# Optimization experiments

Hardware: AMD Instinct MI355X
Metric: run time of the kernel (lower is better)

Reference implementation:

```python
import jax, jax.numpy as jnp
import numpy as np


def setup_inputs() -> dict:
    key = jax.random.key(0)
    ks = jax.random.split(key, 6)
    B, C, H, W = 8, 64, 64, 64
    E = C // 8  # embedding_channels = inChannels // k
    inp = {
        "x": jax.random.normal(ks[0], (B, C, H, W), dtype=jnp.float32),
        "Wk": jax.random.normal(ks[1], (E, C), dtype=jnp.float32) * 0.1,
        "bk": jnp.zeros((E,), dtype=jnp.float32),
        "Wq": jax.random.normal(ks[2], (E, C), dtype=jnp.float32) * 0.1,
        "bq": jnp.zeros((E,), dtype=jnp.float32),
        "Wv": jax.random.normal(ks[3], (E, C), dtype=jnp.float32) * 0.1,
        "bv": jnp.zeros((E,), dtype=jnp.float32),
        "Wo": jax.random.normal(ks[4], (C, E), dtype=jnp.float32) * 0.1,
        "bo": jnp.zeros((C,), dtype=jnp.float32),
        "gamma": jnp.zeros((1,), dtype=jnp.float32),
    }
    return inp


def reference(x, Wk, bk, Wq, bq, Wv, bv, Wo, bo, gamma):
    B, C, H, W = x.shape
    N = H * W
    xf = x.reshape(B, C, N)  # [B, C, N]
    # 1x1 convs are per-pixel linear projections
    f = jnp.einsum('ec,bcn->ben', Wk, xf) + bk[:, None]  # key   [B, E, N]
    g = jnp.einsum('ec,bcn->ben', Wq, xf) + bq[:, None]  # query [B, E, N]
    h = jnp.einsum('ec,bcn->ben', Wv, xf) + bv[:, None]  # value [B, E, N]
    # s = f^T g : [B, N, N]
    s = jnp.einsum('ben,bem->bnm', f, g)
    # softmax over dim=1 (key/row axis) as in the original module
    beta = jax.nn.softmax(s, axis=1)
    v = jnp.einsum('ben,bnm->bem', h, beta)  # [B, E, N]
    o = jnp.einsum('ce,ben->bcn', Wo, v) + bo[:, None]  # [B, C, N]
    o = o.reshape(B, C, H, W)
    y = gamma[0] * o + x
    return (y, o, gamma[0])
```

## Files before the change

### kernel.cpp

```cpp
#include <hip/hip_runtime.h>


#define BB   8
#define CC   64
#define NPIX 4096
#define EE   8
#define BN   (BB*NPIX)
#define YSZ  (BB*CC*NPIX)
#define LOG2E 1.4426950408889634f

typedef __attribute__((ext_vector_type(8))) short bf16x8;
typedef __attribute__((ext_vector_type(4))) float f32x4;

__device__ __forceinline__ unsigned short f2bf_rne(float x) {
    unsigned u = __float_as_uint(x);
    u += 0x7FFFu + ((u >> 16) & 1u);
    return (unsigned short)(u >> 16);
}
__device__ __forceinline__ unsigned pack_bf_trunc(float a, float b) {
    return __builtin_amdgcn_perm(__float_as_uint(b), __float_as_uint(a),
                                 0x07060302u);
}
__device__ __forceinline__ float fexp2(float x) {
    return __int_as_float((int)fmaf(x, 8388608.f, 1065062131.f));
}

__global__ __launch_bounds__(256) void qkv_kernel(
    const float* __restrict__ x,
    const float* __restrict__ Wk, const float* __restrict__ bk,
    const float* __restrict__ Wq, const float* __restrict__ bq,
    const float* __restrict__ Wv, const float* __restrict__ bv,
    unsigned short* __restrict__ QT, unsigned short* __restrict__ KT,
    unsigned short* __restrict__ VT)
{
    const int proj = blockIdx.y;
    const float* W    = (proj == 0) ? Wq : (proj == 1) ? Wk : Wv;
    const float* bias = (proj == 0) ? bq : (proj == 1) ? bk : bv;

    const int bm = blockIdx.x*256 + threadIdx.x;
    const int b  = bm >> 12;
    const int n  = bm & (NPIX-1);
    const float* xb = x + (size_t)b*CC*NPIX + n;

    float xv[CC];
    #pragma unroll
    for (int c = 0; c < CC; ++c) xv[c] = xb[(size_t)c*NPIX];

    float f[EE];
    #pragma unroll
    for (int e = 0; e < EE; ++e) {
        float acc = bias[e];
        #pragma unroll
        for (int c = 0; c < CC; ++c) acc = fmaf(W[e*CC+c], xv[c], acc);
        f[e] = acc;
    }

    if (proj == 0) {
        union { unsigned short s[8]; uint4 v; } t;
        #pragma unroll
        for (int e = 0; e < EE; ++e) t.s[e] = f2bf_rne(f[e] * LOG2E);
        *(uint4*)(QT + (size_t)bm*EE) = t.v;
    } else if (proj == 1) {
        union { unsigned short s[8]; uint4 v; } t;
        #pragma unroll
        for (int e = 0; e < EE; ++e) t.s[e] = f2bf_rne(f[e]);
        *(uint4*)(KT + (size_t)bm*EE) = t.v;
    } else {
        const int p   = n >> 5;
        const int c   = n & 31;
        const int off = ((c & 15) >> 2)*8 + ((c >> 4) << 2) + (c & 3);
        unsigned short* vp = VT + ((size_t)(b*128 + p)*16)*32 + off;
        #pragma unroll
        for (int e = 0; e < EE; ++e) vp[e*32] = f2bf_rne(f[e]);
        vp[8*32] = 0x3F80;
    }
}

__global__ __launch_bounds__(256, 2) void attn_fused(
    const unsigned short* __restrict__ QT, const unsigned short* __restrict__ KT,
    const unsigned short* __restrict__ VT,
    const float* __restrict__ x, const float* __restrict__ Wo,
    const float* __restrict__ bo, const float* __restrict__ gamma,
    float* __restrict__ out)
{
    __shared__ float OB[3*4*256];
    __shared__ float VL[64*13];
    __shared__ float Wos[CC*9];
    __shared__ float bos[CC];

    const int tid  = threadIdx.x;
    const int wave = tid >> 6, lane = tid & 63;
    const int quad = lane >> 4, lm = lane & 15;
    const int b  = blockIdx.x >> 6;
    const int m0 = (blockIdx.x & 63) * 64;

    for (int i = tid; i < CC*EE; i += 256) Wos[(i>>3)*9 + (i&7)] = Wo[i];
    if (tid < CC) bos[tid] = bo[tid];

    const bf16x8 kz = {0,0,0,0,0,0,0,0};
    bf16x8 qf[4][4];
    #pragma unroll
    for (int t = 0; t < 4; ++t) {
        bf16x8 qt = *(const bf16x8*)(QT + (size_t)(b*NPIX + m0 + 16*t + lm)*EE);
        #pragma unroll
        for (int g = 0; g < 4; ++g) qf[t][g] = (quad == g) ? qt : kz;
    }

    f32x4 oacc[4];
    #pragma unroll
    for (int t = 0; t < 4; ++t) oacc[t] = (f32x4){0.f,0.f,0.f,0.f};
    const f32x4 zc = {0.f,0.f,0.f,0.f};

    const unsigned short* Kb = KT + (size_t)b*NPIX*EE;
    const int n_start = wave*1024;
    const unsigned short* kl = Kb + (size_t)(n_start + lane)*EE;
    const int lmv = (lm < 9) ? lm : 8;
    const unsigned short* vl = VT + ((size_t)(b*128 + (n_start >> 5))*16 + lmv)*32
                                  + quad*8;

    bf16x8 kfa  = *(const bf16x8*)(kl);
    bf16x8 vf0a = *(const bf16x8*)(vl);
    bf16x8 vf1a = *(const bf16x8*)(vl + 512);
    bf16x8 kfb  = *(const bf16x8*)(kl + 64*EE);
    bf16x8 vf0b = *(const bf16x8*)(vl + 1024);
    bf16x8 vf1b = *(const bf16x8*)(vl + 1536);
    kl += 128*EE; vl += 2048;

    for (int ch = 0; ch < 16; ++ch) {
        bf16x8 kf = kfa, vf0 = vf0a, vf1 = vf1a;
        kfa = kfb; vf0a = vf0b; vf1a = vf1b;
        if (ch < 14) {
            kfb  = *(const bf16x8*)(kl);
            vf0b = *(const bf16x8*)(vl);
            vf1b = *(const bf16x8*)(vl + 512);
            kl += 64*EE; vl += 1024;
        }

        #pragma unroll
        for (int t = 0; t < 4; ++t) {
            f32x4 s0 = __builtin_amdgcn_mfma_f32_16x16x32_bf16(kf, qf[t][0], zc, 0, 0, 0);
            f32x4 s1 = __builtin_amdgcn_mfma_f32_16x16x32_bf16(kf, qf[t][1], zc, 0, 0, 0);
            f32x4 s2 = __builtin_amdgcn_mfma_f32_16x16x32_bf16(kf, qf[t][2], zc, 0, 0, 0);
            f32x4 s3 = __builtin_amdgcn_mfma_f32_16x16x32_bf16(kf, qf[t][3], zc, 0, 0, 0);

            float a0 = fexp2(s0.x), a1 = fexp2(s0.y);
            float a2 = fexp2(s0.z), a3 = fexp2(s0.w);
            float a4 = fexp2(s1.x), a5 = fexp2(s1.y);
            float a6 = fexp2(s1.z), a7 = fexp2(s1.w);
            float c0 = fexp2(s2.x), c1 = fexp2(s2.y);
            float c2 = fexp2(s2.z), c3 = fexp2(s2.w);
            float c4 = fexp2(s3.x), c5 = fexp2(s3.y);
            float c6 = fexp2(s3.z), c7 = fexp2(s3.w);

            union { unsigned u[4]; bf16x8 v; } p0, p1;
            p0.u[0] = pack_bf_trunc(a0, a1); p0.u[1] = pack_bf_trunc(a2, a3);
            p0.u[2] = pack_bf_trunc(a4, a5); p0.u[3] = pack_bf_trunc(a6, a7);
            p1.u[0] = pack_bf_trunc(c0, c1); p1.u[1] = pack_bf_trunc(c2, c3);
            p1.u[2] = pack_bf_trunc(c4, c5); p1.u[3] = pack_bf_trunc(c6, c7);
            oacc[t] = __builtin_amdgcn_mfma_f32_16x16x32_bf16(vf0, p0.v, oacc[t], 0, 0, 0);
            oacc[t] = __builtin_amdgcn_mfma_f32_16x16x32_bf16(vf1, p1.v, oacc[t], 0, 0, 0);
        }
    }

    if (wave != 0) {
        #pragma unroll
        for (int t = 0; t < 4; ++t)
            *(f32x4*)(OB + ((size_t)(wave-1)*4 + t)*256 + lane*4) = oacc[t];
    }
    __syncthreads();
    if (wave == 0) {
        #pragma unroll
        for (int t = 0; t < 4; ++t) {
            f32x4 oT = oacc[t];
            #pragma unroll
            for (int w = 0; w < 3; ++w)
                oT += *(f32x4*)(OB + ((size_t)w*4 + t)*256 + lane*4);
            float lT  = __shfl(oT.x, 32 + lm);
            float inv = 1.f / lT;
            if (quad < 2) {
                f32x4 sT = { oT.x*inv, oT.y*inv, oT.z*inv, oT.w*inv };
                *(f32x4*)(VL + (16*t + lm)*13 + quad*4) = sT;
            }
        }
    }
    __syncthreads();

    const float g  = gamma[0];
    const int   px = tid & 63;
    const int   cg = tid >> 6;
    const size_t base = (size_t)b*CC*NPIX + (m0 + px);
    float v[EE];
    #pragma unroll
    for (int e = 0; e < EE; ++e) v[e] = VL[px*13 + e];
    #pragma unroll
    for (int i = 0; i < 16; ++i) {
        const int c = cg*16 + i;
        float o = bos[c];
        #pragma unroll
        for (int e = 0; e < EE; ++e) o += Wos[c*9 + e] * v[e];
        out[(size_t)YSZ + base + (size_t)c*NPIX] = o;
        out[base + (size_t)c*NPIX] = g*o + x[base + (size_t)c*NPIX];
    }
    if (blockIdx.x == 0 && tid == 0) out[2*(size_t)YSZ] = g;
}

extern "C" void kernel_launch(void* const* d_in, const int* in_sizes, int n_in,
                              void* d_out, int out_size, void* d_ws, size_t ws_size,
                              hipStream_t stream) {
    const float* x     = (const float*)d_in[0];
    const float* Wk    = (const float*)d_in[1];
    const float* bk    = (const float*)d_in[2];
    const float* Wq    = (const float*)d_in[3];
    const float* bq    = (const float*)d_in[4];
    const float* Wv    = (const float*)d_in[5];
    const float* bv    = (const float*)d_in[6];
    const float* Wo    = (const float*)d_in[7];
    const float* bo    = (const float*)d_in[8];
    const float* gamma = (const float*)d_in[9];
    float* out = (float*)d_out;

    unsigned short* QT = (unsigned short*)d_ws;
    unsigned short* KT = QT + (size_t)BN*EE;
    unsigned short* VT = KT + (size_t)BN*EE;

    qkv_kernel<<<dim3(BN/256, 3), 256, 0, stream>>>(x, Wk, bk, Wq, bq, Wv, bv, QT, KT, VT);
    attn_fused<<<BB*64, 256, 0, stream>>>(QT, KT, VT, x, Wo, bo, gamma, out);
}
```

Baseline: 107.9 us.

## Split attention key range over eight waves and merge QKV projections per block

The attention kernel now runs 512 threads per block, so eight waves each cover 512 keys instead of four waves covering 1024. The partial accumulators are reduced through shared memory by four waves in parallel, and the epilogue is split across more threads. The QKV kernel computes all three projections in one block, one wave per projection, so each x column is loaded by one block and the weight pointers are made wave-uniform with readfirstlane. Q fragments are now selected inside the loop instead of being held as 16 masked registers, which trades fewer registers for extra selects. More waves per block should hide latency better, at the cost of a larger shared buffer and a heavier reduction.

```diff
diff --git a/kernel.cpp b/kernel.cpp
--- a/kernel.cpp
+++ b/kernel.cpp
@@ -24,8 +24,14 @@
 __device__ __forceinline__ float fexp2(float x) {
     return __int_as_float((int)fmaf(x, 8388608.f, 1065062131.f));
 }
-
-__global__ __launch_bounds__(256) void qkv_kernel(
+__device__ __forceinline__ const float* rfl_ptr(const float* p) {
+    unsigned long long u = (unsigned long long)p;
+    unsigned lo = __builtin_amdgcn_readfirstlane((unsigned)u);
+    unsigned hi = __builtin_amdgcn_readfirstlane((unsigned)(u >> 32));
+    return (const float*)(((unsigned long long)hi << 32) | lo);
+}
+
+__global__ __launch_bounds__(192) void qkv_kernel(
     const float* __restrict__ x,
     const float* __restrict__ Wk, const float* __restrict__ bk,
     const float* __restrict__ Wq, const float* __restrict__ bq,
@@ -33,11 +39,12 @@
     unsigned short* __restrict__ QT, unsigned short* __restrict__ KT,
     unsigned short* __restrict__ VT)
 {
-    const int proj = blockIdx.y;
-    const float* W    = (proj == 0) ? Wq : (proj == 1) ? Wk : Wv;
-    const float* bias = (proj == 0) ? bq : (proj == 1) ? bk : bv;
-
-    const int bm = blockIdx.x*256 + threadIdx.x;
+    const int proj = threadIdx.x >> 6;
+    const int lane = threadIdx.x & 63;
+    const float* W    = rfl_ptr((proj == 0) ? Wq : (proj == 1) ? Wk : Wv);
+    const float* bias = rfl_ptr((proj == 0) ? bq : (proj == 1) ? bk : bv);
+
+    const int bm = blockIdx.x*64 + lane;
     const int b  = bm >> 12;
     const int n  = bm & (NPIX-1);
     const float* xb = x + (size_t)b*CC*NPIX + n;
@@ -76,14 +83,14 @@
     }
 }
 
-__global__ __launch_bounds__(256, 2) void attn_fused(
+__global__ __launch_bounds__(512, 4) void attn_fused(
     const unsigned short* __restrict__ QT, const unsigned short* __restrict__ KT,
     const unsigned short* __restrict__ VT,
     const float* __restrict__ x, const float* __restrict__ Wo,
     const float* __restrict__ bo, const float* __restrict__ gamma,
     float* __restrict__ out)
 {
-    __shared__ float OB[3*4*256];
+    __shared__ float OB[8*4*256];
     __shared__ float VL[64*13];
     __shared__ float Wos[CC*9];
     __shared__ float bos[CC];
@@ -94,17 +101,14 @@
     const int b  = blockIdx.x >> 6;
     const int m0 = (blockIdx.x & 63) * 64;
 
-    for (int i = tid; i < CC*EE; i += 256) Wos[(i>>3)*9 + (i&7)] = Wo[i];
+    for (int i = tid; i < CC*EE; i += 512) Wos[(i>>3)*9 + (i&7)] = Wo[i];
     if (tid < CC) bos[tid] = bo[tid];
 
     const bf16x8 kz = {0,0,0,0,0,0,0,0};
-    bf16x8 qf[4][4];
-    #pragma unroll
-    for (int t = 0; t < 4; ++t) {
-        bf16x8 qt = *(const bf16x8*)(QT + (size_t)(b*NPIX + m0 + 16*t + lm)*EE);
-        #pragma unroll
-        for (int g = 0; g < 4; ++g) qf[t][g] = (quad == g) ? qt : kz;
-    }
+    bf16x8 qt[4];
+    #pragma unroll
+    for (int t = 0; t < 4; ++t)
+        qt[t] = *(const bf16x8*)(QT + (size_t)(b*NPIX + m0 + 16*t + lm)*EE);
 
     f32x4 oacc[4];
     #pragma unroll
@@ -112,7 +116,7 @@
     const f32x4 zc = {0.f,0.f,0.f,0.f};
 
     const unsigned short* Kb = KT + (size_t)b*NPIX*EE;
-    const int n_start = wave*1024;
+    const int n_start = wave*512;
     const unsigned short* kl = Kb + (size_t)(n_start + lane)*EE;
     const int lmv = (lm < 9) ? lm : 8;
     const unsigned short* vl = VT + ((size_t)(b*128 + (n_start >> 5))*16 + lmv)*32
@@ -126,10 +130,11 @@
     bf16x8 vf1b = *(const bf16x8*)(vl + 1536);
     kl += 128*EE; vl += 2048;
 
-    for (int ch = 0; ch < 16; ++ch) {
+    #pragma unroll 2
+    for (int ch = 0; ch < 8; ++ch) {
         bf16x8 kf = kfa, vf0 = vf0a, vf1 = vf1a;
         kfa = kfb; vf0a = vf0b; vf1a = vf1b;
-        if (ch < 14) {
+        if (ch < 6) {
             kfb  = *(const bf16x8*)(kl);
             vf0b = *(const bf16x8*)(vl);
             vf1b = *(const bf16x8*)(vl + 512);
@@ -138,10 +143,14 @@
 
         #pragma unroll
         for (int t = 0; t < 4; ++t) {
-            f32x4 s0 = __builtin_amdgcn_mfma_f32_16x16x32_bf16(kf, qf[t][0], zc, 0, 0, 0);
-            f32x4 s1 = __builtin_amdgcn_mfma_f32_16x16x32_bf16(kf, qf[t][1], zc, 0, 0, 0);
-            f32x4 s2 = __builtin_amdgcn_mfma_f32_16x16x32_bf16(kf, qf[t][2], zc, 0, 0, 0);
-            f32x4 s3 = __builtin_amdgcn_mfma_f32_16x16x32_bf16(kf, qf[t][3], zc, 0, 0, 0);
+            f32x4 s0 = __builtin_amdgcn_mfma_f32_16x16x32_bf16(
+                           kf, (quad == 0) ? qt[t] : kz, zc, 0, 0, 0);
+            f32x4 s1 = __builtin_amdgcn_mfma_f32_16x16x32_bf16(
+                           kf, (quad == 1) ? qt[t] : kz, zc, 0, 0, 0);
+            f32x4 s2 = __builtin_amdgcn_mfma_f32_16x16x32_bf16(
+                           kf, (quad == 2) ? qt[t] : kz, zc, 0, 0, 0);
+            f32x4 s3 = __builtin_amdgcn_mfma_f32_16x16x32_bf16(
+                           kf, (quad == 3) ? qt[t] : kz, zc, 0, 0, 0);
 
             float a0 = fexp2(s0.x), a1 = fexp2(s0.y);
             float a2 = fexp2(s0.z), a3 = fexp2(s0.w);
@@ -162,25 +171,21 @@
         }
     }
 
-    if (wave != 0) {
-        #pragma unroll
-        for (int t = 0; t < 4; ++t)
-            *(f32x4*)(OB + ((size_t)(wave-1)*4 + t)*256 + lane*4) = oacc[t];
-    }
+    #pragma unroll
+    for (int t = 0; t < 4; ++t)
+        *(f32x4*)(OB + ((size_t)wave*4 + t)*256 + lane*4) = oacc[t];
     __syncthreads();
-    if (wave == 0) {
-        #pragma unroll
-        for (int t = 0; t < 4; ++t) {
-            f32x4 oT = oacc[t];
-            #pragma unroll
-            for (int w = 0; w < 3; ++w)
-                oT += *(f32x4*)(OB + ((size_t)w*4 + t)*256 + lane*4);
-            float lT  = __shfl(oT.x, 32 + lm);
-            float inv = 1.f / lT;
-            if (quad < 2) {
-                f32x4 sT = { oT.x*inv, oT.y*inv, oT.z*inv, oT.w*inv };
-                *(f32x4*)(VL + (16*t + lm)*13 + quad*4) = sT;
-            }
+    if (wave < 4) {
+        const int t = wave;
+        f32x4 oT = {0.f,0.f,0.f,0.f};
+        #pragma unroll
+        for (int w = 0; w < 8; ++w)
+            oT += *(f32x4*)(OB + ((size_t)w*4 + t)*256 + lane*4);
+        float lT  = __shfl(oT.x, 32 + lm);
+        float inv = 1.f / lT;
+        if (quad < 2) {
+            f32x4 sT = { oT.x*inv, oT.y*inv, oT.z*inv, oT.w*inv };
+            *(f32x4*)(VL + (16*t + lm)*13 + quad*4) = sT;
         }
     }
     __syncthreads();
@@ -193,8 +198,8 @@
     #pragma unroll
     for (int e = 0; e < EE; ++e) v[e] = VL[px*13 + e];
     #pragma unroll
-    for (int i = 0; i < 16; ++i) {
-        const int c = cg*16 + i;
+    for (int i = 0; i < 8; ++i) {
+        const int c = cg*8 + i;
         float o = bos[c];
         #pragma unroll
         for (int e = 0; e < EE; ++e) o += Wos[c*9 + e] * v[e];
@@ -223,6 +228,6 @@
     unsigned short* KT = QT + (size_t)BN*EE;
     unsigned short* VT = KT + (size_t)BN*EE;
 
-    qkv_kernel<<<dim3(BN/256, 3), 256, 0, stream>>>(x, Wk, bk, Wq, bq, Wv, bv, QT, KT, VT);
-    attn_fused<<<BB*64, 256, 0, stream>>>(QT, KT, VT, x, Wo, bo, gamma, out);
-}
+    qkv_kernel<<<BN/64, 192, 0, stream>>>(x, Wk, bk, Wq, bq, Wv, bv, QT, KT, VT);
+    attn_fused<<<BB*64, 512, 0, stream>>>(QT, KT, VT, x, Wo, bo, gamma, out);
+}
```

New measurement: 118.6 us. 9.9% more time.
